# Kernel optimization log

Measured on AMD Instinct MI355X. Metric: run time of the kernel, lower is better.

Reference implementation:

```python
import jax, jax.numpy as jnp
import numpy as np

ROPE_BASE = 10000.0


def _rope_cos_sin(n, d, dtype):
    # standard llama-style rotary embedding over head dim d
    inv_freq = 1.0 / (ROPE_BASE ** (jnp.arange(0, d, 2, dtype=jnp.float32) / d))
    t = jnp.arange(n, dtype=jnp.float32)
    freqs = jnp.einsum('n,f->nf', t, inv_freq)          # [N, d/2]
    emb = jnp.concatenate([freqs, freqs], axis=-1)      # [N, d]
    return jnp.cos(emb).astype(dtype), jnp.sin(emb).astype(dtype)


def _rotate_half(x):
    x1, x2 = jnp.split(x, 2, axis=-1)
    return jnp.concatenate([-x2, x1], axis=-1)


def _apply_rope(x, cos, sin):
    # x: [B, H, N, D]; cos/sin: [N, D] broadcast over B, H
    return x * cos + _rotate_half(x) * sin


def setup_inputs() -> dict:
    key = jax.random.key(0)
    k1, k2, k3 = jax.random.split(key, 3)
    B, N, dim = 2, 2048, 1024
    heads, dim_head = 16, 64
    inner = heads * dim_head
    x = jax.random.normal(k1, (B, N, dim), dtype=jnp.float32)
    w_qkv = jax.random.normal(k2, (dim, 3 * inner), dtype=jnp.float32) * (dim ** -0.5)
    w_out = jax.random.normal(k3, (inner, dim), dtype=jnp.float32) * (inner ** -0.5)
    return {"x": x, "w_qkv": w_qkv, "w_out": w_out}


def reference(x, w_qkv, w_out):
    B, N, _ = x.shape
    heads, dim_head = 16, 64
    qkv = jnp.einsum('bnd,de->bne', x, w_qkv)
    q, k, v = jnp.split(qkv, 3, axis=-1)
    def to_heads(t):
        return t.reshape(B, N, heads, dim_head).transpose(0, 2, 1, 3)  # [B,H,N,D]
    q, k, v = to_heads(q), to_heads(k), to_heads(v)
    cos, sin = _rope_cos_sin(N, dim_head, x.dtype)
    q = _apply_rope(q, cos, sin)
    k = _apply_rope(k, cos, sin)
    scale = dim_head ** -0.5
    scores = jnp.einsum('bhqd,bhkd->bhqk', q, k) * scale   # [B,H,N,N], non-causal
    attn = jax.nn.softmax(scores, axis=-1)
    out = jnp.einsum('bhqk,bhkd->bhqd', attn, v)
    out = out.transpose(0, 2, 1, 3).reshape(B, N, heads * dim_head)
    return jnp.einsum('bne,ed->bnd', out, w_out)
```

## Files before the change

### kernel.cpp

```cpp
#include <hip/hip_runtime.h>

typedef __attribute__((ext_vector_type(8))) short bf16x8;
typedef __attribute__((ext_vector_type(4))) short bf16x4;
typedef __attribute__((ext_vector_type(4))) float f32x4;

#define MFMA(a, b, c) __builtin_amdgcn_mfma_f32_16x16x32_bf16(a, b, c, 0, 0, 0)
#define MFMA16(a, b, c) __builtin_amdgcn_mfma_f32_16x16x16bf16_1k(a, b, c, 0, 0, 0)

__device__ __forceinline__ unsigned short f2bf(float f) {
    unsigned u = __builtin_bit_cast(unsigned, f);
    u += 0x7fffu + ((u >> 16) & 1u);
    return (unsigned short)(u >> 16);
}

__device__ __forceinline__ void gload16(const unsigned short* g, unsigned short* l) {
    __builtin_amdgcn_global_load_lds(
        (const __attribute__((address_space(1))) void*)g,
        (__attribute__((address_space(3))) void*)l, 16, 0, 0);
}

__device__ __forceinline__ unsigned pack_bf16(float lo, float hi) {
    unsigned a = __builtin_bit_cast(unsigned, lo) + 0x8000u;
    unsigned b = __builtin_bit_cast(unsigned, hi) + 0x8000u;
    return __builtin_amdgcn_perm(b, a, 0x07060302);
}
__device__ __forceinline__ unsigned pack_bf16_trunc(float lo, float hi) {
    return __builtin_amdgcn_perm(__builtin_bit_cast(unsigned, hi),
                                 __builtin_bit_cast(unsigned, lo), 0x07060302);
}


__global__ __launch_bounds__(256) void cvt_bf16(const float* __restrict__ in,
                                                unsigned short* __restrict__ out, int n) {
    int i = (blockIdx.x * 256 + threadIdx.x) * 4;
    if (i < n) {
        float4 f = *(const float4*)(in + i);
        ushort4 u;
        u.x = f2bf(f.x); u.y = f2bf(f.y); u.z = f2bf(f.z); u.w = f2bf(f.w);
        *(ushort4*)(out + i) = u;
    }
}

__global__ __launch_bounds__(256) void transpose_cvt(const float* __restrict__ in,
                                                     unsigned short* __restrict__ out,
                                                     int R, int C) {
    __shared__ float tile[32][33];
    const int c0 = blockIdx.x * 32, r0 = blockIdx.y * 32;
    const int tr = threadIdx.x >> 3;
    const int j4 = (threadIdx.x & 7) * 4;
    float4 f = *(const float4*)(in + (size_t)(r0 + tr) * C + c0 + j4);
    tile[tr][j4 + 0] = f.x; tile[tr][j4 + 1] = f.y;
    tile[tr][j4 + 2] = f.z; tile[tr][j4 + 3] = f.w;
    __syncthreads();
    ushort4 u;
    u.x = f2bf(tile[j4 + 0][tr]); u.y = f2bf(tile[j4 + 1][tr]);
    u.z = f2bf(tile[j4 + 2][tr]); u.w = f2bf(tile[j4 + 3][tr]);
    *(ushort4*)(out + (size_t)(c0 + tr) * R + r0 + j4) = u;
}

__global__ __launch_bounds__(256) void rope_tab(float* __restrict__ cosT,
                                                float* __restrict__ sinT) {
    int i = blockIdx.x * 256 + threadIdx.x;
    int n = i >> 5, f = i & 31;
    float ang = (float)n * exp2f((float)f * -0.4152410118609203f);
    float s, c;
    sincosf(ang, &s, &c);
    cosT[i] = c; sinT[i] = s;
}


template <int EPI>
__global__ __launch_bounds__(256, 3) void gemm_bt(const unsigned short* __restrict__ A,
                                                  const unsigned short* __restrict__ Bt,
                                                  int K, int Ncols,
                                                  unsigned short* __restrict__ oq,
                                                  unsigned short* __restrict__ ok,
                                                  unsigned short* __restrict__ ovt,
                                                  float* __restrict__ of,
                                                  const float* __restrict__ cosT,
                                                  const float* __restrict__ sinT) {
    __shared__ unsigned short As[2][128 * 32];
    __shared__ unsigned short Bs[2][128 * 32];
    const int tid = threadIdx.x;
    const int w = tid >> 6, lane = tid & 63, quad = lane >> 4, cc = lane & 15;
    const int wm = w >> 1, wn = w & 1;
    const int m0 = blockIdx.y * 128, n0 = blockIdx.x * 128;

    size_t aoff[2], boff[2];
#pragma unroll
    for (int t = 0; t < 2; t++) {
        int S = w * 128 + t * 64 + lane;
        int row = S >> 2;
        int c = (S & 3) ^ ((row >> 1) & 3);
        aoff[t] = (size_t)(m0 + row) * K + c * 8;
        boff[t] = (size_t)(n0 + row) * K + c * 8;
    }

#pragma unroll
    for (int t = 0; t < 2; t++) {
        gload16(A + aoff[t], &As[0][(w * 2 + t) * 512]);
        gload16(Bt + boff[t], &Bs[0][(w * 2 + t) * 512]);
    }
    __syncthreads();

    f32x4 acc[4][4] = {};
    const int rpos = (quad ^ ((cc >> 1) & 3)) * 8;
    const int nkt = K >> 5;

    for (int kt = 0; kt < nkt; kt++) {
        const int pb = kt & 1;
        if (kt < nkt - 1) {
            const int ko = (kt + 1) * 32;
#pragma unroll
            for (int t = 0; t < 2; t++) {
                gload16(A + aoff[t] + ko, &As[pb ^ 1][(w * 2 + t) * 512]);
                gload16(Bt + boff[t] + ko, &Bs[pb ^ 1][(w * 2 + t) * 512]);
            }
        }
        bf16x8 af[4], bf[4];
#pragma unroll
        for (int i = 0; i < 4; i++)
            af[i] = *(const bf16x8*)&As[pb][(wm * 64 + i * 16 + cc) * 32 + rpos];
#pragma unroll
        for (int i = 0; i < 4; i++)
            bf[i] = *(const bf16x8*)&Bs[pb][(wn * 64 + i * 16 + cc) * 32 + rpos];
#pragma unroll
        for (int i = 0; i < 4; i++)
#pragma unroll
            for (int j = 0; j < 4; j++)
                acc[i][j] = MFMA(af[i], bf[j], acc[i][j]);
        __syncthreads();
    }

    if (EPI == 0) {
        const int e0 = n0 + wn * 64;
        const int which = e0 >> 10;
        const int h = (e0 >> 6) & 15;
        if (which < 2) {
            unsigned short* dst = (which == 0) ? oq : ok;
            const float postscale = (which == 0) ? 0.18033688f : 1.0f;
#pragma unroll
            for (int mf = 0; mf < 4; mf++) {
#pragma unroll
                for (int r = 0; r < 4; r++) {
                    int mg = m0 + wm * 64 + mf * 16 + quad * 4 + r;
                    int nseq = mg & 2047, b = mg >> 11;
                    float vals[4];
#pragma unroll
                    for (int nf = 0; nf < 4; nf++) vals[nf] = acc[mf][nf][r];
                    size_t rowbase = ((size_t)(b * 16 + h) * 2048 + nseq) * 64;
#pragma unroll
                    for (int nf = 0; nf < 4; nf++) {
                        int d = nf * 16 + cc;
                        int f = d & 31;
                        float cs = cosT[nseq * 32 + f];
                        float sn = sinT[nseq * 32 + f];
                        float partner = vals[nf ^ 2];
                        float outv = (vals[nf] * cs +
                                      ((nf < 2) ? -partner : partner) * sn) * postscale;
                        dst[rowbase + d] = f2bf(outv);
                    }
                }
            }
        } else {
#pragma unroll
            for (int mf = 0; mf < 4; mf++) {
                int mg0 = m0 + wm * 64 + mf * 16 + quad * 4;
                int b = mg0 >> 11, nseq = mg0 & 2047;
#pragma unroll
                for (int nf = 0; nf < 4; nf++) {
                    int d = nf * 16 + cc;
                    ushort4 pk;
                    pk.x = f2bf(acc[mf][nf][0]);
                    pk.y = f2bf(acc[mf][nf][1]);
                    pk.z = f2bf(acc[mf][nf][2]);
                    pk.w = f2bf(acc[mf][nf][3]);
                    *(ushort4*)(ovt + ((size_t)(b * 16 + h) * 64 + d) * 2048 + nseq) = pk;
                }
            }
        }
    } else {
#pragma unroll
        for (int mf = 0; mf < 4; mf++)
#pragma unroll
            for (int nf = 0; nf < 4; nf++)
#pragma unroll
                for (int r = 0; r < 4; r++) {
                    int mg = m0 + wm * 64 + mf * 16 + quad * 4 + r;
                    of[(size_t)mg * Ncols + n0 + wn * 64 + nf * 16 + cc] = acc[mf][nf][r];
                }
    }
}


__global__ __launch_bounds__(256, 4) void attn_half(const unsigned short* __restrict__ q,
                                                    const unsigned short* __restrict__ k,
                                                    const unsigned short* __restrict__ vt,
                                                    unsigned short* __restrict__ opart,
                                                    float* __restrict__ rspart) {
    __shared__ unsigned short ks[2][64 * 64];
    __shared__ unsigned short vs[2][64 * 64];
    const int tid = threadIdx.x;
    const int w = tid >> 6, lane = tid & 63, quad = lane >> 4, cc = lane & 15;
    const int bh = blockIdx.x & 31;
    const int half = (blockIdx.x >> 5) & 1;
    const int qt = blockIdx.x >> 6;

    const unsigned short* qg = q + ((size_t)bh * 2048 + qt * 128 + w * 32) * 64;
    bf16x8 aq[2][2];
#pragma unroll
    for (int mf = 0; mf < 2; mf++)
#pragma unroll
        for (int kc = 0; kc < 2; kc++)
            aq[mf][kc] = *(const bf16x8*)(qg + (mf * 16 + cc) * 64 + kc * 32 + quad * 8);

    int koff[2], voff[2];
#pragma unroll
    for (int t = 0; t < 2; t++) {
        int S = w * 128 + t * 64 + lane;
        int row = S >> 3;
        int c = (S & 7) ^ (row & 7);
        koff[t] = row * 64 + c * 8;
        voff[t] = row * 2048 + c * 8;
    }

    const unsigned short* kg0 = k + (size_t)bh * 2048 * 64 + half * 65536;
    const unsigned short* vg0 = vt + (size_t)bh * 64 * 2048 + half * 1024;

#pragma unroll
    for (int t = 0; t < 2; t++) {
        gload16(kg0 + koff[t], &ks[0][(w * 2 + t) * 512]);
        gload16(vg0 + voff[t], &vs[0][(w * 2 + t) * 512]);
    }
    __syncthreads();

    f32x4 oacc[2][4] = {};
    float rs[2] = {};

    for (int kt = 0; kt < 16; kt++) {
        const int pb = kt & 1;
        if (kt < 15) {
            const unsigned short* kb = kg0 + (kt + 1) * 4096;
            const unsigned short* vb = vg0 + (kt + 1) * 64;
#pragma unroll
            for (int t = 0; t < 2; t++) {
                gload16(kb + koff[t], &ks[pb ^ 1][(w * 2 + t) * 512]);
                gload16(vb + voff[t], &vs[pb ^ 1][(w * 2 + t) * 512]);
            }
        }

        f32x4 s2[2][4] = {};
#pragma unroll
        for (int kc = 0; kc < 2; kc++) {
#pragma unroll
            for (int nf = 0; nf < 4; nf++) {
                bf16x8 bk = *(const bf16x8*)&ks[pb][(nf * 16 + cc) * 64 +
                                                    ((kc * 4 + quad) ^ (cc & 7)) * 8];
                s2[0][nf] = MFMA(bk, aq[0][kc], s2[0][nf]);
                s2[1][nf] = MFMA(bk, aq[1][kc], s2[1][nf]);
            }
        }

        bf16x4 pkr[2][4];
#pragma unroll
        for (int mf = 0; mf < 2; mf++) {
#pragma unroll
            for (int nf = 0; nf < 4; nf++) {
                float p0 = __builtin_amdgcn_exp2f(s2[mf][nf][0]);
                float p1 = __builtin_amdgcn_exp2f(s2[mf][nf][1]);
                float p2 = __builtin_amdgcn_exp2f(s2[mf][nf][2]);
                float p3 = __builtin_amdgcn_exp2f(s2[mf][nf][3]);
                rs[mf] += (p0 + p1) + (p2 + p3);
                uint2 u;
                u.x = pack_bf16_trunc(p0, p1);
                u.y = pack_bf16_trunc(p2, p3);
                pkr[mf][nf] = __builtin_bit_cast(bf16x4, u);
            }
        }

#pragma unroll
        for (int nf = 0; nf < 4; nf++) {
#pragma unroll
            for (int df = 0; df < 4; df++) {
                bf16x4 bv = *(const bf16x4*)&vs[pb][(df * 16 + cc) * 64 +
                                                    (((nf * 2 + (quad >> 1)) ^ (cc & 7)) * 8) +
                                                    (quad & 1) * 4];
                oacc[0][df] = MFMA16(bv, pkr[0][nf], oacc[0][df]);
                oacc[1][df] = MFMA16(bv, pkr[1][nf], oacc[1][df]);
            }
        }

        __syncthreads();
    }

#pragma unroll
    for (int mf = 0; mf < 2; mf++) {
        rs[mf] += __shfl_xor(rs[mf], 16, 64);
        rs[mf] += __shfl_xor(rs[mf], 32, 64);
    }

    {
        unsigned short* op = opart +
            ((size_t)(half * 32 + bh) * 2048 + qt * 128 + w * 32) * 64;
#pragma unroll
        for (int mf = 0; mf < 2; mf++)
#pragma unroll
            for (int df = 0; df < 4; df++) {
                uint2 u;
                u.x = pack_bf16(oacc[mf][df][0], oacc[mf][df][1]);
                u.y = pack_bf16(oacc[mf][df][2], oacc[mf][df][3]);
                *(uint2*)(op + (size_t)(mf * 16 + cc) * 64 + df * 16 + quad * 4) = u;
            }
        if (lane < 16) {
            float* rp = rspart + (size_t)(half * 32 + bh) * 2048 + qt * 128 + w * 32;
            rp[cc] = rs[0];
            rp[16 + cc] = rs[1];
        }
    }
}

__global__ __launch_bounds__(256) void attn_combine(const unsigned short* __restrict__ opart,
                                                    const float* __restrict__ rspart,
                                                    unsigned short* __restrict__ o) {
    int i = blockIdx.x * 256 + threadIdx.x;
    int base = i * 8;
    int bh = base >> 17, m = (base >> 6) & 2047, d0 = base & 63;
    const unsigned short* o1 = opart + base;
    const unsigned short* o2 = opart + 32 * 2048 * 64 + base;
    float r = rspart[(bh << 11) + m] + rspart[(32 << 11) + (bh << 11) + m];
    float inv = 1.0f / r;
    ushort4 a0 = *(const ushort4*)o1, a1 = *(const ushort4*)(o1 + 4);
    ushort4 b0 = *(const ushort4*)o2, b1 = *(const ushort4*)(o2 + 4);
    unsigned short res[8];
    const unsigned short* ap = (const unsigned short*)&a0;
    const unsigned short* bp = (const unsigned short*)&b0;
#pragma unroll
    for (int j = 0; j < 8; j++) {
        unsigned short av = (j < 4) ? ((const unsigned short*)&a0)[j]
                                    : ((const unsigned short*)&a1)[j - 4];
        unsigned short bv = (j < 4) ? ((const unsigned short*)&b0)[j]
                                    : ((const unsigned short*)&b1)[j - 4];
        float fa = __builtin_bit_cast(float, (unsigned)av << 16);
        float fb = __builtin_bit_cast(float, (unsigned)bv << 16);
        res[j] = f2bf((fa + fb) * inv);
    }
    unsigned short* dst = o + ((size_t)((bh >> 4) * 2048 + m)) * 1024 + (bh & 15) * 64 + d0;
    *(ushort4*)dst = *(const ushort4*)&res[0];
    *(ushort4*)(dst + 4) = *(const ushort4*)&res[4];
    (void)ap; (void)bp;
}


extern "C" void kernel_launch(void* const* d_in, const int* in_sizes, int n_in,
                              void* d_out, int out_size, void* d_ws, size_t ws_size,
                              hipStream_t stream) {
    const float* x = (const float*)d_in[0];
    const float* w_qkv = (const float*)d_in[1];
    const float* w_out = (const float*)d_in[2];
    float* out = (float*)d_out;

    unsigned short* xb    = (unsigned short*)d_ws;
    unsigned short* wqkvT = xb + 4096 * 1024;
    unsigned short* woutT = wqkvT + 3072 * 1024;
    unsigned short* qb    = woutT + 1024 * 1024;
    unsigned short* kb    = qb + 2 * 16 * 2048 * 64;
    unsigned short* vtb   = kb + 2 * 16 * 2048 * 64;
    unsigned short* ob    = vtb + 2 * 16 * 2048 * 64;
    float* cosT = (float*)(ob + 4096 * 1024);
    float* sinT = cosT + 2048 * 32;
    unsigned short* opart = (unsigned short*)(sinT + 2048 * 32);
    float* rspart = (float*)(opart + 2 * 32 * 2048 * 64);

    rope_tab<<<256, 256, 0, stream>>>(cosT, sinT);
    cvt_bf16<<<4096, 256, 0, stream>>>(x, xb, 4096 * 1024);
    transpose_cvt<<<dim3(96, 32), 256, 0, stream>>>(w_qkv, wqkvT, 1024, 3072);
    transpose_cvt<<<dim3(32, 32), 256, 0, stream>>>(w_out, woutT, 1024, 1024);
    gemm_bt<0><<<dim3(24, 32), 256, 0, stream>>>(xb, wqkvT, 1024, 3072,
                                                 qb, kb, vtb, nullptr, cosT, sinT);
    attn_half<<<1024, 256, 0, stream>>>(qb, kb, vtb, opart, rspart);
    attn_combine<<<2048, 256, 0, stream>>>(opart, rspart, ob);
    gemm_bt<1><<<dim3(8, 32), 256, 0, stream>>>(ob, woutT, 1024, 1024,
                                                nullptr, nullptr, nullptr, out,
                                                nullptr, nullptr);
}
```

Measured before the change: 191.7 us.

## Split attention keys into quarters and fuse prep kernels into one launch

The attention kernel now splits the key sequence into four parts instead of two. Each block processes 32-key tiles with smaller shared buffers and a higher occupancy hint, which gives 2048 blocks instead of 1024 to fill the GPU. The combine kernel now sums four partial outputs and row sums, which adds extra memory traffic for the bf16 partials. Separately, the three prep kernels (x conversion, weight transposes, rope table) are merged into one launch to cut launch overhead.

```diff
diff --git a/kernel.cpp b/kernel.cpp
--- a/kernel.cpp
+++ b/kernel.cpp
@@ -30,42 +30,53 @@
 }
 
 
-__global__ __launch_bounds__(256) void cvt_bf16(const float* __restrict__ in,
-                                                unsigned short* __restrict__ out, int n) {
-    int i = (blockIdx.x * 256 + threadIdx.x) * 4;
-    if (i < n) {
-        float4 f = *(const float4*)(in + i);
+__global__ __launch_bounds__(256) void prep(const float* __restrict__ x,
+                                            const float* __restrict__ wqkv,
+                                            const float* __restrict__ wout,
+                                            unsigned short* __restrict__ xb,
+                                            unsigned short* __restrict__ wqkvT,
+                                            unsigned short* __restrict__ woutT,
+                                            float* __restrict__ cosT,
+                                            float* __restrict__ sinT) {
+    __shared__ float tile[32][33];
+    const int bid = blockIdx.x, tid = threadIdx.x;
+    if (bid < 4096) {
+        int i = (bid * 256 + tid) * 4;
+        float4 f = *(const float4*)(x + i);
         ushort4 u;
         u.x = f2bf(f.x); u.y = f2bf(f.y); u.z = f2bf(f.z); u.w = f2bf(f.w);
-        *(ushort4*)(out + i) = u;
-    }
-}
-
-__global__ __launch_bounds__(256) void transpose_cvt(const float* __restrict__ in,
-                                                     unsigned short* __restrict__ out,
-                                                     int R, int C) {
-    __shared__ float tile[32][33];
-    const int c0 = blockIdx.x * 32, r0 = blockIdx.y * 32;
-    const int tr = threadIdx.x >> 3;
-    const int j4 = (threadIdx.x & 7) * 4;
-    float4 f = *(const float4*)(in + (size_t)(r0 + tr) * C + c0 + j4);
-    tile[tr][j4 + 0] = f.x; tile[tr][j4 + 1] = f.y;
-    tile[tr][j4 + 2] = f.z; tile[tr][j4 + 3] = f.w;
-    __syncthreads();
-    ushort4 u;
-    u.x = f2bf(tile[j4 + 0][tr]); u.y = f2bf(tile[j4 + 1][tr]);
-    u.z = f2bf(tile[j4 + 2][tr]); u.w = f2bf(tile[j4 + 3][tr]);
-    *(ushort4*)(out + (size_t)(c0 + tr) * R + r0 + j4) = u;
-}
-
-__global__ __launch_bounds__(256) void rope_tab(float* __restrict__ cosT,
-                                                float* __restrict__ sinT) {
-    int i = blockIdx.x * 256 + threadIdx.x;
-    int n = i >> 5, f = i & 31;
-    float ang = (float)n * exp2f((float)f * -0.4152410118609203f);
-    float s, c;
-    sincosf(ang, &s, &c);
-    cosT[i] = c; sinT[i] = s;
+        *(ushort4*)(xb + i) = u;
+    } else if (bid < 8448 - 256) {
+        const float* tin; unsigned short* tout;
+        int R, C, bx, by;
+        if (bid < 4096 + 3072) {
+            int idx = bid - 4096;
+            tin = wqkv; tout = wqkvT; R = 1024; C = 3072;
+            bx = idx % 96; by = idx / 96;
+        } else {
+            int idx = bid - 7168;
+            tin = wout; tout = woutT; R = 1024; C = 1024;
+            bx = idx & 31; by = idx >> 5;
+        }
+        const int c0 = bx * 32, r0 = by * 32;
+        const int tr = tid >> 3;
+        const int j4 = (tid & 7) * 4;
+        float4 f = *(const float4*)(tin + (size_t)(r0 + tr) * C + c0 + j4);
+        tile[tr][j4 + 0] = f.x; tile[tr][j4 + 1] = f.y;
+        tile[tr][j4 + 2] = f.z; tile[tr][j4 + 3] = f.w;
+        __syncthreads();
+        ushort4 u;
+        u.x = f2bf(tile[j4 + 0][tr]); u.y = f2bf(tile[j4 + 1][tr]);
+        u.z = f2bf(tile[j4 + 2][tr]); u.w = f2bf(tile[j4 + 3][tr]);
+        *(ushort4*)(tout + (size_t)(c0 + tr) * R + r0 + j4) = u;
+    } else {
+        int i = (bid - 8192) * 256 + tid;
+        int n = i >> 5, f = i & 31;
+        float ang = (float)n * exp2f((float)f * -0.4152410118609203f);
+        float s, c;
+        sincosf(ang, &s, &c);
+        cosT[i] = c; sinT[i] = s;
+    }
 }
 
 
@@ -193,18 +204,18 @@
 }
 
 
-__global__ __launch_bounds__(256, 4) void attn_half(const unsigned short* __restrict__ q,
-                                                    const unsigned short* __restrict__ k,
-                                                    const unsigned short* __restrict__ vt,
-                                                    unsigned short* __restrict__ opart,
-                                                    float* __restrict__ rspart) {
-    __shared__ unsigned short ks[2][64 * 64];
-    __shared__ unsigned short vs[2][64 * 64];
+__global__ __launch_bounds__(256, 6) void attn_quarter(const unsigned short* __restrict__ q,
+                                                       const unsigned short* __restrict__ k,
+                                                       const unsigned short* __restrict__ vt,
+                                                       unsigned short* __restrict__ opart,
+                                                       float* __restrict__ rspart) {
+    __shared__ unsigned short ks[2][32 * 64];
+    __shared__ unsigned short vs[2][64 * 32];
     const int tid = threadIdx.x;
     const int w = tid >> 6, lane = tid & 63, quad = lane >> 4, cc = lane & 15;
     const int bh = blockIdx.x & 31;
-    const int half = (blockIdx.x >> 5) & 1;
-    const int qt = blockIdx.x >> 6;
+    const int qt = (blockIdx.x >> 5) & 15;
+    const int quarter = blockIdx.x >> 9;
 
     const unsigned short* qg = q + ((size_t)bh * 2048 + qt * 128 + w * 32) * 64;
     bf16x8 aq[2][2];
@@ -214,24 +225,17 @@
         for (int kc = 0; kc < 2; kc++)
             aq[mf][kc] = *(const bf16x8*)(qg + (mf * 16 + cc) * 64 + kc * 32 + quad * 8);
 
-    int koff[2], voff[2];
-#pragma unroll
-    for (int t = 0; t < 2; t++) {
-        int S = w * 128 + t * 64 + lane;
-        int row = S >> 3;
-        int c = (S & 7) ^ (row & 7);
-        koff[t] = row * 64 + c * 8;
-        voff[t] = row * 2048 + c * 8;
-    }
-
-    const unsigned short* kg0 = k + (size_t)bh * 2048 * 64 + half * 65536;
-    const unsigned short* vg0 = vt + (size_t)bh * 64 * 2048 + half * 1024;
-
-#pragma unroll
-    for (int t = 0; t < 2; t++) {
-        gload16(kg0 + koff[t], &ks[0][(w * 2 + t) * 512]);
-        gload16(vg0 + voff[t], &vs[0][(w * 2 + t) * 512]);
-    }
+    const int S = w * 64 + lane;
+    const int krow = S >> 3, kc_ = (S & 7) ^ (krow & 7);
+    const int koff = krow * 64 + kc_ * 8;
+    const int vrow = S >> 2, vc_ = (S & 3) ^ (vrow & 3);
+    const int voff = vrow * 2048 + vc_ * 8;
+
+    const unsigned short* kg0 = k + (size_t)bh * 131072 + quarter * 32768;
+    const unsigned short* vg0 = vt + (size_t)bh * 131072 + quarter * 512;
+
+    gload16(kg0 + koff, &ks[0][w * 512]);
+    gload16(vg0 + voff, &vs[0][w * 512]);
     __syncthreads();
 
     f32x4 oacc[2][4] = {};
@@ -240,20 +244,15 @@
     for (int kt = 0; kt < 16; kt++) {
         const int pb = kt & 1;
         if (kt < 15) {
-            const unsigned short* kb = kg0 + (kt + 1) * 4096;
-            const unsigned short* vb = vg0 + (kt + 1) * 64;
-#pragma unroll
-            for (int t = 0; t < 2; t++) {
-                gload16(kb + koff[t], &ks[pb ^ 1][(w * 2 + t) * 512]);
-                gload16(vb + voff[t], &vs[pb ^ 1][(w * 2 + t) * 512]);
-            }
-        }
-
-        f32x4 s2[2][4] = {};
+            gload16(kg0 + (kt + 1) * 2048 + koff, &ks[pb ^ 1][w * 512]);
+            gload16(vg0 + (kt + 1) * 32 + voff, &vs[pb ^ 1][w * 512]);
+        }
+
+        f32x4 s2[2][2] = {};
 #pragma unroll
         for (int kc = 0; kc < 2; kc++) {
 #pragma unroll
-            for (int nf = 0; nf < 4; nf++) {
+            for (int nf = 0; nf < 2; nf++) {
                 bf16x8 bk = *(const bf16x8*)&ks[pb][(nf * 16 + cc) * 64 +
                                                     ((kc * 4 + quad) ^ (cc & 7)) * 8];
                 s2[0][nf] = MFMA(bk, aq[0][kc], s2[0][nf]);
@@ -261,11 +260,11 @@
             }
         }
 
-        bf16x4 pkr[2][4];
+        bf16x4 pkr[2][2];
 #pragma unroll
         for (int mf = 0; mf < 2; mf++) {
 #pragma unroll
-            for (int nf = 0; nf < 4; nf++) {
+            for (int nf = 0; nf < 2; nf++) {
                 float p0 = __builtin_amdgcn_exp2f(s2[mf][nf][0]);
                 float p1 = __builtin_amdgcn_exp2f(s2[mf][nf][1]);
                 float p2 = __builtin_amdgcn_exp2f(s2[mf][nf][2]);
@@ -279,11 +278,11 @@
         }
 
 #pragma unroll
-        for (int nf = 0; nf < 4; nf++) {
+        for (int nf = 0; nf < 2; nf++) {
 #pragma unroll
             for (int df = 0; df < 4; df++) {
-                bf16x4 bv = *(const bf16x4*)&vs[pb][(df * 16 + cc) * 64 +
-                                                    (((nf * 2 + (quad >> 1)) ^ (cc & 7)) * 8) +
+                bf16x4 bv = *(const bf16x4*)&vs[pb][(df * 16 + cc) * 32 +
+                                                    (((nf * 2 + (quad >> 1)) ^ (cc & 3)) * 8) +
                                                     (quad & 1) * 4];
                 oacc[0][df] = MFMA16(bv, pkr[0][nf], oacc[0][df]);
                 oacc[1][df] = MFMA16(bv, pkr[1][nf], oacc[1][df]);
@@ -301,7 +300,7 @@
 
     {
         unsigned short* op = opart +
-            ((size_t)(half * 32 + bh) * 2048 + qt * 128 + w * 32) * 64;
+            ((size_t)(quarter * 32 + bh) * 2048 + qt * 128 + w * 32) * 64;
 #pragma unroll
         for (int mf = 0; mf < 2; mf++)
 #pragma unroll
@@ -312,7 +311,7 @@
                 *(uint2*)(op + (size_t)(mf * 16 + cc) * 64 + df * 16 + quad * 4) = u;
             }
         if (lane < 16) {
-            float* rp = rspart + (size_t)(half * 32 + bh) * 2048 + qt * 128 + w * 32;
+            float* rp = rspart + (size_t)(quarter * 32 + bh) * 2048 + qt * 128 + w * 32;
             rp[cc] = rs[0];
             rp[16 + cc] = rs[1];
         }
@@ -325,29 +324,29 @@
     int i = blockIdx.x * 256 + threadIdx.x;
     int base = i * 8;
     int bh = base >> 17, m = (base >> 6) & 2047, d0 = base & 63;
-    const unsigned short* o1 = opart + base;
-    const unsigned short* o2 = opart + 32 * 2048 * 64 + base;
-    float r = rspart[(bh << 11) + m] + rspart[(32 << 11) + (bh << 11) + m];
+    float r = 0.0f;
+#pragma unroll
+    for (int qq = 0; qq < 4; qq++) r += rspart[qq * 65536 + (bh << 11) + m];
     float inv = 1.0f / r;
-    ushort4 a0 = *(const ushort4*)o1, a1 = *(const ushort4*)(o1 + 4);
-    ushort4 b0 = *(const ushort4*)o2, b1 = *(const ushort4*)(o2 + 4);
+    float acc[8] = {};
+#pragma unroll
+    for (int qq = 0; qq < 4; qq++) {
+        const unsigned short* op = opart + (size_t)qq * 4194304 + base;
+        ushort4 a0 = *(const ushort4*)op, a1 = *(const ushort4*)(op + 4);
+        const unsigned short* av = (const unsigned short*)&a0;
+        const unsigned short* bv = (const unsigned short*)&a1;
+#pragma unroll
+        for (int j = 0; j < 4; j++) {
+            acc[j] += __builtin_bit_cast(float, (unsigned)av[j] << 16);
+            acc[4 + j] += __builtin_bit_cast(float, (unsigned)bv[j] << 16);
+        }
+    }
     unsigned short res[8];
-    const unsigned short* ap = (const unsigned short*)&a0;
-    const unsigned short* bp = (const unsigned short*)&b0;
-#pragma unroll
-    for (int j = 0; j < 8; j++) {
-        unsigned short av = (j < 4) ? ((const unsigned short*)&a0)[j]
-                                    : ((const unsigned short*)&a1)[j - 4];
-        unsigned short bv = (j < 4) ? ((const unsigned short*)&b0)[j]
-                                    : ((const unsigned short*)&b1)[j - 4];
-        float fa = __builtin_bit_cast(float, (unsigned)av << 16);
-        float fb = __builtin_bit_cast(float, (unsigned)bv << 16);
-        res[j] = f2bf((fa + fb) * inv);
-    }
+#pragma unroll
+    for (int j = 0; j < 8; j++) res[j] = f2bf(acc[j] * inv);
     unsigned short* dst = o + ((size_t)((bh >> 4) * 2048 + m)) * 1024 + (bh & 15) * 64 + d0;
     *(ushort4*)dst = *(const ushort4*)&res[0];
     *(ushort4*)(dst + 4) = *(const ushort4*)&res[4];
-    (void)ap; (void)bp;
 }
 
 
@@ -369,15 +368,12 @@
     float* cosT = (float*)(ob + 4096 * 1024);
     float* sinT = cosT + 2048 * 32;
     unsigned short* opart = (unsigned short*)(sinT + 2048 * 32);
-    float* rspart = (float*)(opart + 2 * 32 * 2048 * 64);
-
-    rope_tab<<<256, 256, 0, stream>>>(cosT, sinT);
-    cvt_bf16<<<4096, 256, 0, stream>>>(x, xb, 4096 * 1024);
-    transpose_cvt<<<dim3(96, 32), 256, 0, stream>>>(w_qkv, wqkvT, 1024, 3072);
-    transpose_cvt<<<dim3(32, 32), 256, 0, stream>>>(w_out, woutT, 1024, 1024);
+    float* rspart = (float*)(opart + 4 * 32 * 2048 * 64);
+
+    prep<<<8448, 256, 0, stream>>>(x, w_qkv, w_out, xb, wqkvT, woutT, cosT, sinT);
     gemm_bt<0><<<dim3(24, 32), 256, 0, stream>>>(xb, wqkvT, 1024, 3072,
                                                  qb, kb, vtb, nullptr, cosT, sinT);
-    attn_half<<<1024, 256, 0, stream>>>(qb, kb, vtb, opart, rspart);
+    attn_quarter<<<2048, 256, 0, stream>>>(qb, kb, vtb, opart, rspart);
     attn_combine<<<2048, 256, 0, stream>>>(opart, rspart, ob);
     gemm_bt<1><<<dim3(8, 32), 256, 0, stream>>>(ob, woutT, 1024, 1024,
                                                 nullptr, nullptr, nullptr, out,
```

After: 232.6 us. +21.4%, slower.
